# Kernel tuning notes

Measured on AMD Instinct MI355X. Metric: run time of the kernel, lower is better.

Reference implementation:

```python
import jax, jax.numpy as jnp
import numpy as np

B, IN, H, OUT = 4096, 1024, 2048, 1024
EPS = 1e-5  # added to std (not variance), matching the torch module


def _ln(z, a, b):
    # torch.std default is unbiased (ddof=1); eps added to sigma
    mu = jnp.mean(z, axis=1, keepdims=True)
    sigma = jnp.std(z, axis=1, ddof=1, keepdims=True)
    return (z - mu) / (sigma + EPS) * a + b


def setup_inputs() -> dict:
    key = jax.random.key(0)
    ks = iter(jax.random.split(key, 40))
    W = lambda i, o: (jax.random.normal(next(ks), (o, i), jnp.float32) / np.sqrt(i)).astype(jnp.float32)
    bz = lambda o: jnp.zeros((o,), jnp.float32)
    d = {
        "inp": jax.random.normal(next(ks), (B, IN), jnp.float32),
        "h_0": jax.random.normal(next(ks), (B, H), jnp.float32),
        "c_0": jax.random.normal(next(ks), (B, H), jnp.float32),
        # h-side gate linears (H -> H)
        "Wfh": W(H, H), "bfh": bz(H), "Wih": W(H, H), "bih": bz(H),
        "Wch": W(H, H), "bch": bz(H), "Woh": W(H, H), "boh": bz(H),
        # x-side gate linears (IN -> H)
        "Wfx": W(IN, H), "bfx": bz(H), "Wix": W(IN, H), "bix": bz(H),
        "Wcx": W(IN, H), "bcx": bz(H), "Wox": W(IN, H), "box": bz(H),
        # decoder (H -> OUT)
        "Wdec": W(H, OUT), "bdec": bz(OUT),
        # LayerNormalization params (a2 ones, b2 zeros), shape (1, H)
        "ax": jnp.ones((1, H), jnp.float32), "bx": jnp.zeros((1, H), jnp.float32),
        "ah": jnp.ones((1, H), jnp.float32), "bh": jnp.zeros((1, H), jnp.float32),
        "ac": jnp.ones((1, H), jnp.float32), "bc": jnp.zeros((1, H), jnp.float32),
    }
    return d


def reference(inp, h_0, c_0,
              Wfh, bfh, Wih, bih, Wch, bch, Woh, boh,
              Wfx, bfx, Wix, bix, Wcx, bcx, Wox, box,
              Wdec, bdec, ax, bx, ah, bh, ac, bc):
    lin = lambda x, W, b: x @ W.T + b
    gate = lambda wx, bx_, wh, bh_: (_ln(lin(inp, wx, bx_), ax, bx)
                                     + _ln(lin(h_0, wh, bh_), ah, bh))
    f_g = jax.nn.sigmoid(gate(Wfx, bfx, Wfh, bfh))
    i_g = jax.nn.sigmoid(gate(Wix, bix, Wih, bih))
    c_tilda = jnp.tanh(gate(Wcx, bcx, Wch, bch))
    cx = f_g * c_0 + i_g * c_tilda
    o_g = jax.nn.sigmoid(gate(Wox, box, Woh, boh))
    hx = o_g * jnp.tanh(_ln(cx, ac, bc))
    out = lin(hx, Wdec, bdec)  # decoder applied to hidden state (vectorized over batch)
    return (out, hx, cx)
```

## Files before the change

### kernel.cpp

```cpp
#include <hip/hip_runtime.h>

#define NB   4096
#define NIN  1024
#define NH   2048
#define NOUT 1024
#define NH4  8192

typedef short short8 __attribute__((ext_vector_type(8)));
typedef float f32x4 __attribute__((ext_vector_type(4)));
typedef float f32x16 __attribute__((ext_vector_type(16)));
typedef unsigned short ushort8v __attribute__((ext_vector_type(8)));

__device__ __forceinline__ float bf2f(unsigned short u) {
  union { unsigned int i; float f; } c; c.i = ((unsigned int)u) << 16; return c.f;
}
__device__ __forceinline__ unsigned short f2bf(float f) {
  union { float f; unsigned int i; } c; c.f = f;
  unsigned int u = c.i;
  u += 0x7FFFu + ((u >> 16) & 1u);
  return (unsigned short)(u >> 16);
}
__device__ __forceinline__ float sigf(float x) { return 1.0f / (1.0f + __expf(-x)); }
__device__ __forceinline__ float tanh_f(float x) { return 1.0f - 2.0f / (__expf(2.0f * x) + 1.0f); }

#define CNT_INP  ((size_t)NB * NIN)
#define CNT_H0   ((size_t)NB * NH)
#define CNT_WXG  ((size_t)NH * NIN)
#define CNT_WHG  ((size_t)NH * NH)
#define CNT_WD   ((size_t)NOUT * NH)
#define OFF_XB   ((size_t)0)
#define OFF_H0B  (OFF_XB + CNT_INP)
#define OFF_HXB  (OFF_H0B + CNT_H0)
#define OFF_WX   (OFF_HXB + CNT_H0)
#define OFF_WH   (OFF_WX + 4 * CNT_WXG)
#define OFF_WD   (OFF_WH + 4 * CNT_WHG)
#define OFF_ZX   (OFF_WD + CNT_WD)
#define OFF_ZH   (OFF_ZX + (size_t)NB * NH4)
#define CVT_TOTAL (OFF_WD + CNT_WD)

struct CvtArgs { const float* src[11]; };

__global__ __launch_bounds__(256) void cvt_all(CvtArgs a, unsigned short* __restrict__ dstBase) {
  const size_t i = ((size_t)blockIdx.x * 256 + threadIdx.x) * 8;
  if (i >= CVT_TOTAL) return;
  const size_t cnt[11] = {CNT_INP, CNT_H0, CNT_WXG, CNT_WXG, CNT_WXG, CNT_WXG,
                          CNT_WHG, CNT_WHG, CNT_WHG, CNT_WHG, CNT_WD};
  const size_t dst[11] = {OFF_XB, OFF_H0B,
                          OFF_WX, OFF_WX + CNT_WXG, OFF_WX + 2 * CNT_WXG, OFF_WX + 3 * CNT_WXG,
                          OFF_WH, OFF_WH + CNT_WHG, OFF_WH + 2 * CNT_WHG, OFF_WH + 3 * CNT_WHG,
                          OFF_WD};
  size_t base = 0;
#pragma unroll
  for (int s = 0; s < 11; s++) {
    if (i < base + cnt[s]) {
      const size_t off = i - base;
      const float* sp = a.src[s] + off;
      float4 v0 = *(const float4*)(sp);
      float4 v1 = *(const float4*)(sp + 4);
      ushort8v o;
      o[0] = f2bf(v0.x); o[1] = f2bf(v0.y); o[2] = f2bf(v0.z); o[3] = f2bf(v0.w);
      o[4] = f2bf(v1.x); o[5] = f2bf(v1.y); o[6] = f2bf(v1.z); o[7] = f2bf(v1.w);
      *(ushort8v*)(dstBase + dst[s] + off) = o;
      return;
    }
    base += cnt[s];
  }
}

__device__ __forceinline__ void gload16(const void* g, void* l) {
  __builtin_amdgcn_global_load_lds((const __attribute__((address_space(1))) void*)g,
                                   (__attribute__((address_space(3))) void*)l, 16, 0, 0);
}

#define SCH0  __builtin_amdgcn_sched_barrier(0)
#define BARR  __builtin_amdgcn_s_barrier()
#define LGKM0 asm volatile("s_waitcnt lgkmcnt(0)" ::: "memory")
#define VMC6  asm volatile("s_waitcnt vmcnt(6)" ::: "memory")
#define VMC0  asm volatile("s_waitcnt vmcnt(0)" ::: "memory")

__global__ __launch_bounds__(512) void gemm_dual8(
    const unsigned short* __restrict__ Xb, const unsigned short* __restrict__ Wx,
    const unsigned short* __restrict__ H0b, const unsigned short* __restrict__ Wh,
    const float* bx0, const float* bx1, const float* bx2, const float* bx3,
    const float* bh0, const float* bh1, const float* bh2, const float* bh3,
    unsigned short* __restrict__ Zx, unsigned short* __restrict__ Zh) {
  __shared__ __align__(16) unsigned short As[2][256 * 64];
  __shared__ __align__(16) unsigned short Bs[2][256 * 64];

  const unsigned short* Ag; const unsigned short* Bg;
  const float *p0, *p1, *p2, *p3; unsigned short* Cg; int K;
  if (blockIdx.z == 0) { Ag = Xb;  Bg = Wx; Cg = Zx; K = NIN; p0 = bx0; p1 = bx1; p2 = bx2; p3 = bx3; }
  else                 { Ag = H0b; Bg = Wh; Cg = Zh; K = NH;  p0 = bh0; p1 = bh1; p2 = bh2; p3 = bh3; }

  const int t    = threadIdx.x;
  const int wid  = t >> 6;
  const int lane = t & 63;
  const int m15  = lane & 15;
  const int g4   = lane >> 4;
  const int wm   = wid >> 2;
  const int wn   = wid & 3;
  const int rloc = lane >> 3;
  const int slot = lane & 7;
  const int ck   = slot ^ rloc ^ ((wid & 3) << 1);
  const int m0   = blockIdx.y * 256;
  const int n0   = blockIdx.x * 256;
  const int NT   = K >> 6;
  const size_t thrOff = (size_t)(wid * 8 + rloc) * K + ck * 8;

#define STAGE_HALF(G, R0, H, TT, LDBASE) do {                                                     \
    const unsigned short* _gs = (G) + thrOff + (size_t)((R0) + (H) * 128) * K + (size_t)(TT) * 64; \
    unsigned short* _ld = (LDBASE) + ((H) * 128 + wid * 8) * 64;                                   \
    gload16(_gs, _ld);                                                                             \
    gload16(_gs + (size_t)64 * K, _ld + 4096);                                                     \
  } while (0)

#define SWZ(R) (((R) & 7) ^ ((((R) >> 3) & 3) << 1))
#define LD8(S, ROW, KC) (*(const short8*)&(S)[(ROW) * 64 + (((KC) ^ SWZ(ROW)) * 8)])

  f32x4 acc[8][4];
#pragma unroll
  for (int m = 0; m < 8; m++)
#pragma unroll
    for (int n = 0; n < 4; n++)
#pragma unroll
      for (int r = 0; r < 4; r++) acc[m][n][r] = 0.f;

  STAGE_HALF(Ag, m0, 0, 0, As[0]);
  STAGE_HALF(Ag, m0, 1, 0, As[0]);
  STAGE_HALF(Bg, n0, 0, 0, Bs[0]);
  STAGE_HALF(Bg, n0, 1, 0, Bs[0]);
  STAGE_HALF(Bg, n0, 0, 1, Bs[1]);
  STAGE_HALF(Bg, n0, 1, 1, Bs[1]);
  STAGE_HALF(Ag, m0, 0, 1, As[1]);
  VMC6;
  SCH0; BARR; SCH0;

  for (int kt = 0; kt < NT; ++kt) {
    const int cur = kt & 1;
    const unsigned short* sA = As[cur];
    const unsigned short* sB = Bs[cur];
    const int tp1 = (kt + 1 < NT) ? kt + 1 : NT - 1;
    const int tp2 = (kt + 2 < NT) ? kt + 2 : NT - 1;
    short8 b[4][2], a[4][2];

#pragma unroll
    for (int n = 0; n < 2; n++) {
      const int row = wn * 64 + n * 16 + m15;
      b[n][0] = LD8(sB, row, g4);
      b[n][1] = LD8(sB, row, 4 + g4);
    }
#pragma unroll
    for (int m = 0; m < 4; m++) {
      const int row = wm * 128 + m * 16 + m15;
      a[m][0] = LD8(sA, row, g4);
      a[m][1] = LD8(sA, row, 4 + g4);
    }
    STAGE_HALF(Ag, m0, 1, tp1, As[cur ^ 1]);
    SCH0; BARR; LGKM0; SCH0;
    __builtin_amdgcn_s_setprio(1);
#pragma unroll
    for (int m = 0; m < 4; m++)
#pragma unroll
      for (int n = 0; n < 2; n++) {
        acc[m][n] = __builtin_amdgcn_mfma_f32_16x16x32_bf16(a[m][0], b[n][0], acc[m][n], 0, 0, 0);
        acc[m][n] = __builtin_amdgcn_mfma_f32_16x16x32_bf16(a[m][1], b[n][1], acc[m][n], 0, 0, 0);
      }
    __builtin_amdgcn_s_setprio(0);
    SCH0; BARR; SCH0;

#pragma unroll
    for (int n = 2; n < 4; n++) {
      const int row = wn * 64 + n * 16 + m15;
      b[n][0] = LD8(sB, row, g4);
      b[n][1] = LD8(sB, row, 4 + g4);
    }
    SCH0; BARR; LGKM0; SCH0;
    __builtin_amdgcn_s_setprio(1);
#pragma unroll
    for (int m = 0; m < 4; m++)
#pragma unroll
      for (int n = 0; n < 2; n++) {
        acc[m][2 + n] = __builtin_amdgcn_mfma_f32_16x16x32_bf16(a[m][0], b[2 + n][0], acc[m][2 + n], 0, 0, 0);
        acc[m][2 + n] = __builtin_amdgcn_mfma_f32_16x16x32_bf16(a[m][1], b[2 + n][1], acc[m][2 + n], 0, 0, 0);
      }
    __builtin_amdgcn_s_setprio(0);
    SCH0; BARR; SCH0;

#pragma unroll
    for (int m = 0; m < 4; m++) {
      const int row = wm * 128 + 64 + m * 16 + m15;
      a[m][0] = LD8(sA, row, g4);
      a[m][1] = LD8(sA, row, 4 + g4);
    }
    STAGE_HALF(Bg, n0, 0, tp2, Bs[cur]);
    SCH0; BARR; LGKM0; SCH0;
    __builtin_amdgcn_s_setprio(1);
#pragma unroll
    for (int m = 0; m < 4; m++)
#pragma unroll
      for (int n = 0; n < 2; n++) {
        acc[4 + m][n] = __builtin_amdgcn_mfma_f32_16x16x32_bf16(a[m][0], b[n][0], acc[4 + m][n], 0, 0, 0);
        acc[4 + m][n] = __builtin_amdgcn_mfma_f32_16x16x32_bf16(a[m][1], b[n][1], acc[4 + m][n], 0, 0, 0);
      }
    __builtin_amdgcn_s_setprio(0);
    SCH0; BARR; SCH0;

    STAGE_HALF(Bg, n0, 1, tp2, Bs[cur]);
    STAGE_HALF(Ag, m0, 0, tp2, As[cur]);
    SCH0; BARR; SCH0;
    __builtin_amdgcn_s_setprio(1);
#pragma unroll
    for (int m = 0; m < 4; m++)
#pragma unroll
      for (int n = 0; n < 2; n++) {
        acc[4 + m][2 + n] = __builtin_amdgcn_mfma_f32_16x16x32_bf16(a[m][0], b[2 + n][0], acc[4 + m][2 + n], 0, 0, 0);
        acc[4 + m][2 + n] = __builtin_amdgcn_mfma_f32_16x16x32_bf16(a[m][1], b[2 + n][1], acc[4 + m][2 + n], 0, 0, 0);
      }
    __builtin_amdgcn_s_setprio(0);
    VMC6;
    SCH0; BARR; SCH0;
  }

  VMC0;
  SCH0; BARR; SCH0;

  {
    unsigned short* wls = &As[0][0] + wid * (16 * 68);
    float bvn[4];
#pragma unroll
    for (int n = 0; n < 4; n++) {
      const int col = n0 + wn * 64 + n * 16 + m15;
      const float* bp = (col < 2048) ? p0 : ((col < 4096) ? p1 : ((col < 6144) ? p2 : p3));
      bvn[n] = bp[col & 2047];
    }
    const int lrow0 = lane >> 3;
    const int lcol0 = (lane & 7) * 8;
#pragma unroll
    for (int mt = 0; mt < 8; mt++) {
#pragma unroll
      for (int n = 0; n < 4; n++)
#pragma unroll
        for (int r = 0; r < 4; r++)
          wls[(g4 * 4 + r) * 68 + n * 16 + m15] = f2bf(acc[mt][n][r] + bvn[n]);
      LGKM0; SCH0;
#pragma unroll
      for (int i = 0; i < 2; i++) {
        const int lrow = i * 8 + lrow0;
        short8 v = *(const short8*)&wls[lrow * 68 + lcol0];
        *(short8*)&Cg[(size_t)(m0 + wm * 128 + mt * 16 + lrow) * NH4 + (n0 + wn * 64 + lcol0)] = v;
      }
      LGKM0; SCH0;
    }
  }
#undef STAGE_HALF
#undef SWZ
#undef LD8
}

template<int MT, bool BOUT>
__device__ __forceinline__ void gemm_core32(const unsigned short* __restrict__ A,
                                            const unsigned short* __restrict__ Bm,
                                            const float* b0p, const float* b1p,
                                            const float* b2p, const float* b3p,
                                            float* __restrict__ Cf, unsigned short* __restrict__ Cb,
                                            int N, int K) {
  constexpr int TM = MT * 64;
  __shared__ __align__(16) unsigned short As[TM * 64];
  __shared__ __align__(16) unsigned short Bs[128 * 64];
  const int t = threadIdx.x;
  const int w = t >> 6;
  const int lane = t & 63;
  const int r31 = lane & 31;
  const int hi = lane >> 5;
  const int rloc = lane >> 3;
  const int slot = lane & 7;
  const int m0 = blockIdx.y * TM;
  const int n0 = blockIdx.x * 128;
  const int wm = (w >> 1) * (MT * 32);
  const int wn = (w & 1) * 64;

  f32x16 acc[MT][2];
#pragma unroll
  for (int i = 0; i < MT; i++)
#pragma unroll
    for (int j = 0; j < 2; j++)
#pragma unroll
      for (int r = 0; r < 16; r++) acc[i][j][r] = 0.f;

  const unsigned short* AgP[2 * MT];
  unsigned short* AsP[2 * MT];
#pragma unroll
  for (int q = 0; q < 2 * MT; q++) {
    const int iss = w + 4 * q;
    const int bblk = slot ^ rloc ^ (iss & 3);
    AgP[q] = A + (size_t)(m0 + iss * 8 + rloc) * K + bblk * 8;
    AsP[q] = As + iss * 512;
  }
  const unsigned short* BgP[4];
  unsigned short* BsP[4];
#pragma unroll
  for (int q = 0; q < 4; q++) {
    const int iss = w + 4 * q;
    const int bblk = slot ^ rloc ^ (iss & 3);
    BgP[q] = Bm + (size_t)(n0 + iss * 8 + rloc) * K + bblk * 8;
    BsP[q] = Bs + iss * 512;
  }

  const int swz = (r31 & 7) ^ ((r31 >> 3) & 3);

  for (int k0 = 0; k0 < K; k0 += 64) {
#pragma unroll
    for (int q = 0; q < 2 * MT; q++) gload16(AgP[q] + k0, AsP[q]);
#pragma unroll
    for (int q = 0; q < 4; q++) gload16(BgP[q] + k0, BsP[q]);
    __syncthreads();

#pragma unroll
    for (int ks = 0; ks < 4; ks++) {
      const int phys = ((ks * 2 + hi) ^ swz) * 8;
      short8 af[MT], bf[2];
#pragma unroll
      for (int mt = 0; mt < MT; mt++) af[mt] = *(const short8*)&As[(wm + mt * 32 + r31) * 64 + phys];
#pragma unroll
      for (int jt = 0; jt < 2; jt++) bf[jt] = *(const short8*)&Bs[(wn + jt * 32 + r31) * 64 + phys];
#pragma unroll
      for (int mt = 0; mt < MT; mt++)
#pragma unroll
        for (int jt = 0; jt < 2; jt++)
          acc[mt][jt] = __builtin_amdgcn_mfma_f32_32x32x16_bf16(af[mt], bf[jt], acc[mt][jt], 0, 0, 0);
    }
    __syncthreads();
  }

#pragma unroll
  for (int mt = 0; mt < MT; mt++) {
#pragma unroll
    for (int jt = 0; jt < 2; jt++) {
      const int col = n0 + wn + jt * 32 + r31;
      const float* bp = (col < 2048) ? b0p : ((col < 4096) ? b1p : ((col < 6144) ? b2p : b3p));
      const float bv = bp[col & 2047];
      const int rowb = m0 + wm + mt * 32 + hi * 4;
#pragma unroll
      for (int reg = 0; reg < 16; reg++) {
        const int row = rowb + (reg & 3) + 8 * (reg >> 2);
        const float v = acc[mt][jt][reg] + bv;
        const size_t idx = (size_t)row * N + col;
        if (BOUT) Cb[idx] = f2bf(v);
        else      Cf[idx] = v;
      }
    }
  }
}

__global__ __launch_bounds__(256) void gemm_dec(const unsigned short* __restrict__ HXb,
                                                const unsigned short* __restrict__ Wd,
                                                const float* __restrict__ bdec,
                                                float* __restrict__ out) {
  gemm_core32<1, false>(HXb, Wd, bdec, bdec, bdec, bdec, out, nullptr, NOUT, NH);
}

__global__ __launch_bounds__(256) void ln_gates(const unsigned short* __restrict__ Zx,
                                                const unsigned short* __restrict__ Zh,
                                                const float* __restrict__ c0,
                                                const float* __restrict__ ax, const float* __restrict__ bx,
                                                const float* __restrict__ ah, const float* __restrict__ bh,
                                                const float* __restrict__ ac, const float* __restrict__ bc,
                                                float* __restrict__ out_top,
                                                unsigned short* __restrict__ hx_bf) {
  const int b = blockIdx.x;
  const int t = threadIdx.x;
  const int n = t * 8;
  const int w = t >> 6;
  const int lane = t & 63;
  const float inv_n = 1.0f / 2048.0f, inv_nm1 = 1.0f / 2047.0f;

  short8 zx[4], zh[4];
  const size_t rowoff = (size_t)b * NH4;
#pragma unroll
  for (int g = 0; g < 4; g++) {
    zx[g] = *(const short8*)(Zx + rowoff + g * NH + n);
    zh[g] = *(const short8*)(Zh + rowoff + g * NH + n);
  }

  float s[16];
#pragma unroll
  for (int g = 0; g < 4; g++) {
    float su = 0, sq = 0, su2 = 0, sq2 = 0;
#pragma unroll
    for (int j = 0; j < 8; j++) {
      float v = bf2f((unsigned short)zx[g][j]); su += v; sq += v * v;
      float u = bf2f((unsigned short)zh[g][j]); su2 += u; sq2 += u * u;
    }
    s[g * 4 + 0] = su; s[g * 4 + 1] = sq; s[g * 4 + 2] = su2; s[g * 4 + 3] = sq2;
  }
#pragma unroll
  for (int i = 0; i < 16; i++) {
    float v = s[i];
#pragma unroll
    for (int o = 32; o > 0; o >>= 1) v += __shfl_xor(v, o, 64);
    s[i] = v;
  }
  __shared__ float red[4][16];
  __shared__ float red2[4][2];
  if (lane == 0) {
#pragma unroll
    for (int i = 0; i < 16; i++) red[w][i] = s[i];
  }
  __syncthreads();
#pragma unroll
  for (int i = 0; i < 16; i++) s[i] = red[0][i] + red[1][i] + red[2][i] + red[3][i];

  float mux[4], ivx[4], muh[4], ivh[4];
#pragma unroll
  for (int g = 0; g < 4; g++) {
    mux[g] = s[g * 4 + 0] * inv_n;
    float vx = fmaxf((s[g * 4 + 1] - s[g * 4 + 0] * mux[g]) * inv_nm1, 0.0f);
    ivx[g] = 1.0f / (sqrtf(vx) + 1e-5f);
    muh[g] = s[g * 4 + 2] * inv_n;
    float vh = fmaxf((s[g * 4 + 3] - s[g * 4 + 2] * muh[g]) * inv_nm1, 0.0f);
    ivh[g] = 1.0f / (sqrtf(vh) + 1e-5f);
  }

  float axl[8], bxl[8], ahl[8], bhl[8], c0l[8];
  *(float4*)&axl[0] = *(const float4*)(ax + n); *(float4*)&axl[4] = *(const float4*)(ax + n + 4);
  *(float4*)&bxl[0] = *(const float4*)(bx + n); *(float4*)&bxl[4] = *(const float4*)(bx + n + 4);
  *(float4*)&ahl[0] = *(const float4*)(ah + n); *(float4*)&ahl[4] = *(const float4*)(ah + n + 4);
  *(float4*)&bhl[0] = *(const float4*)(bh + n); *(float4*)&bhl[4] = *(const float4*)(bh + n + 4);
  const float* c0p = c0 + (size_t)b * NH + n;
  *(float4*)&c0l[0] = *(const float4*)(c0p); *(float4*)&c0l[4] = *(const float4*)(c0p + 4);

  float cx[8], og[8];
  float cs = 0, css = 0;
#pragma unroll
  for (int j = 0; j < 8; j++) {
    float pre[4];
#pragma unroll
    for (int g = 0; g < 4; g++) {
      float vx = bf2f((unsigned short)zx[g][j]);
      float vh = bf2f((unsigned short)zh[g][j]);
      pre[g] = ((vx - mux[g]) * ivx[g]) * axl[j] + bxl[j]
             + ((vh - muh[g]) * ivh[g]) * ahl[j] + bhl[j];
    }
    float fg = sigf(pre[0]);
    float ig = sigf(pre[1]);
    float ct = tanh_f(pre[2]);
    og[j] = sigf(pre[3]);
    float c = fg * c0l[j] + ig * ct;
    cx[j] = c; cs += c; css += c * c;
  }
#pragma unroll
  for (int o = 32; o > 0; o >>= 1) { cs += __shfl_xor(cs, o, 64); css += __shfl_xor(css, o, 64); }
  if (lane == 0) { red2[w][0] = cs; red2[w][1] = css; }
  __syncthreads();
  cs = red2[0][0] + red2[1][0] + red2[2][0] + red2[3][0];
  css = red2[0][1] + red2[1][1] + red2[2][1] + red2[3][1];
  const float muc = cs * inv_n;
  const float varc = fmaxf((css - cs * muc) * inv_nm1, 0.0f);
  const float ivc = 1.0f / (sqrtf(varc) + 1e-5f);

  float acl[8], bcl[8];
  *(float4*)&acl[0] = *(const float4*)(ac + n); *(float4*)&acl[4] = *(const float4*)(ac + n + 4);
  *(float4*)&bcl[0] = *(const float4*)(bc + n); *(float4*)&bcl[4] = *(const float4*)(bc + n + 4);

  float hx[8];
#pragma unroll
  for (int j = 0; j < 8; j++)
    hx[j] = og[j] * tanh_f((cx[j] - muc) * ivc * acl[j] + bcl[j]);

  float* hx_out = out_top + (size_t)NB * NOUT + (size_t)b * NH + n;
  float* cx_out = out_top + (size_t)NB * NOUT + (size_t)NB * NH + (size_t)b * NH + n;
  float4 v;
  v.x = hx[0]; v.y = hx[1]; v.z = hx[2]; v.w = hx[3]; *(float4*)(hx_out) = v;
  v.x = hx[4]; v.y = hx[5]; v.z = hx[6]; v.w = hx[7]; *(float4*)(hx_out + 4) = v;
  v.x = cx[0]; v.y = cx[1]; v.z = cx[2]; v.w = cx[3]; *(float4*)(cx_out) = v;
  v.x = cx[4]; v.y = cx[5]; v.z = cx[6]; v.w = cx[7]; *(float4*)(cx_out + 4) = v;
  ushort8v hb;
#pragma unroll
  for (int j = 0; j < 8; j++) hb[j] = f2bf(hx[j]);
  *(ushort8v*)(hx_bf + (size_t)b * NH + n) = hb;
}

extern "C" void kernel_launch(void* const* d_in, const int* in_sizes, int n_in,
                              void* d_out, int out_size, void* d_ws, size_t ws_size,
                              hipStream_t stream) {
  const float* inp = (const float*)d_in[0];
  const float* h0  = (const float*)d_in[1];
  const float* c0  = (const float*)d_in[2];
  const float* bhg[4] = {(const float*)d_in[4], (const float*)d_in[6], (const float*)d_in[8], (const float*)d_in[10]};
  const float* bxg[4] = {(const float*)d_in[12], (const float*)d_in[14], (const float*)d_in[16], (const float*)d_in[18]};
  const float* bdec = (const float*)d_in[20];
  const float* ax = (const float*)d_in[21];
  const float* bx = (const float*)d_in[22];
  const float* ah = (const float*)d_in[23];
  const float* bh = (const float*)d_in[24];
  const float* ac = (const float*)d_in[25];
  const float* bc = (const float*)d_in[26];

  unsigned short* wsb = (unsigned short*)d_ws;
  unsigned short* Xb   = wsb + OFF_XB;
  unsigned short* H0b  = wsb + OFF_H0B;
  unsigned short* HXb  = wsb + OFF_HXB;
  unsigned short* Wx4b = wsb + OFF_WX;
  unsigned short* Wh4b = wsb + OFF_WH;
  unsigned short* Wdb  = wsb + OFF_WD;
  unsigned short* Zx   = wsb + OFF_ZX;
  unsigned short* Zh   = wsb + OFF_ZH;

  CvtArgs ca;
  ca.src[0] = inp; ca.src[1] = h0;
  ca.src[2] = (const float*)d_in[11]; ca.src[3] = (const float*)d_in[13];
  ca.src[4] = (const float*)d_in[15]; ca.src[5] = (const float*)d_in[17];
  ca.src[6] = (const float*)d_in[3];  ca.src[7] = (const float*)d_in[5];
  ca.src[8] = (const float*)d_in[7];  ca.src[9] = (const float*)d_in[9];
  ca.src[10] = (const float*)d_in[19];
  {
    const size_t nthr = CVT_TOTAL / 8;
    cvt_all<<<dim3((unsigned)((nthr + 255) / 256)), dim3(256), 0, stream>>>(ca, wsb);
  }

  gemm_dual8<<<dim3(NH4 / 256, NB / 256, 2), 512, 0, stream>>>(
      Xb, Wx4b, H0b, Wh4b,
      bxg[0], bxg[1], bxg[2], bxg[3],
      bhg[0], bhg[1], bhg[2], bhg[3],
      Zx, Zh);

  ln_gates<<<dim3(NB), 256, 0, stream>>>(Zx, Zh, c0, ax, bx, ah, bh, ac, bc, (float*)d_out, HXb);

  gemm_dec<<<dim3(NOUT / 128, NB / 64), 256, 0, stream>>>(HXb, Wdb, bdec, (float*)d_out);
}
```

Before: 578.6 us.

## Restructure dual-GEMM main loop with unroll-by-two and finer LDS/MFMA interleaving

The main K loop of gemm_dual8 is unrolled by two with fixed double-buffer indices. Swizzled LDS offsets for the A and B fragments are precomputed once per thread. Each tile step now issues LDS fragment reads in smaller groups between MFMA batches and drops several workgroup barriers and explicit lgkmcnt waits, so LDS reads overlap with matrix math. The risk is that leaving waitcnt placement to the compiler, plus keeping more fragments live at once, raises register pressure or adds hidden stalls.

```diff
diff --git a/kernel.cpp b/kernel.cpp
--- a/kernel.cpp
+++ b/kernel.cpp
@@ -77,6 +77,115 @@
 #define LGKM0 asm volatile("s_waitcnt lgkmcnt(0)" ::: "memory")
 #define VMC6  asm volatile("s_waitcnt vmcnt(6)" ::: "memory")
 #define VMC0  asm volatile("s_waitcnt vmcnt(0)" ::: "memory")
+#define PRIO1 __builtin_amdgcn_s_setprio(1)
+#define PRIO0 __builtin_amdgcn_s_setprio(0)
+#define MFMA16(A, B, C) __builtin_amdgcn_mfma_f32_16x16x32_bf16((A), (B), (C), 0, 0, 0)
+
+#define SWZ(R) (((R) & 7) ^ ((((R) >> 3) & 3) << 1))
+
+
+__device__ __forceinline__ void stage_half(const unsigned short* __restrict__ G, size_t thrOff, int K,
+                                           int R0, int H, int T, unsigned short* __restrict__ ldbase, int wid) {
+  const unsigned short* gs = G + thrOff + (size_t)(R0 + H * 128) * K + (size_t)T * 64;
+  unsigned short* ld = ldbase + (H * 128 + wid * 8) * 64;
+  gload16(gs, ld);
+  gload16(gs + (size_t)64 * K, ld + 4096);
+}
+
+__device__ __forceinline__ void tile_step(
+    const unsigned short* __restrict__ sA, const unsigned short* __restrict__ sB,
+    unsigned short* __restrict__ sAc, unsigned short* __restrict__ sBc, unsigned short* __restrict__ sAn,
+    int t1, int t2,
+    const unsigned short* __restrict__ Ag, const unsigned short* __restrict__ Bg,
+    size_t thrOff, int m0, int n0, int K, int wid,
+    const int (&oA)[8][2], const int (&oB)[4][2], f32x4 (&acc)[8][4]) {
+  short8 b01[2][2], b23[2][2], alo[4][2], ahi[4][2];
+
+#pragma unroll
+  for (int n = 0; n < 2; n++) {
+    b01[n][0] = *(const short8*)&sB[oB[n][0]];
+    b01[n][1] = *(const short8*)&sB[oB[n][1]];
+  }
+#pragma unroll
+  for (int m = 0; m < 2; m++) {
+    alo[m][0] = *(const short8*)&sA[oA[m][0]];
+    alo[m][1] = *(const short8*)&sA[oA[m][1]];
+  }
+  stage_half(Ag, thrOff, K, m0, 1, t1, sAn, wid);
+  SCH0;
+#pragma unroll
+  for (int m = 2; m < 4; m++) {
+    alo[m][0] = *(const short8*)&sA[oA[m][0]];
+    alo[m][1] = *(const short8*)&sA[oA[m][1]];
+  }
+  SCH0;
+  PRIO1;
+#pragma unroll
+  for (int m = 0; m < 2; m++)
+#pragma unroll
+    for (int n = 0; n < 2; n++) {
+      acc[m][n] = MFMA16(alo[m][0], b01[n][0], acc[m][n]);
+      acc[m][n] = MFMA16(alo[m][1], b01[n][1], acc[m][n]);
+    }
+  PRIO0; SCH0;
+#pragma unroll
+  for (int n = 0; n < 2; n++) {
+    b23[n][0] = *(const short8*)&sB[oB[2 + n][0]];
+    b23[n][1] = *(const short8*)&sB[oB[2 + n][1]];
+  }
+  SCH0;
+  PRIO1;
+#pragma unroll
+  for (int m = 2; m < 4; m++)
+#pragma unroll
+    for (int n = 0; n < 2; n++) {
+      acc[m][n] = MFMA16(alo[m][0], b01[n][0], acc[m][n]);
+      acc[m][n] = MFMA16(alo[m][1], b01[n][1], acc[m][n]);
+    }
+  PRIO0; SCH0;
+#pragma unroll
+  for (int m = 0; m < 4; m++) {
+    ahi[m][0] = *(const short8*)&sA[oA[4 + m][0]];
+    ahi[m][1] = *(const short8*)&sA[oA[4 + m][1]];
+  }
+  SCH0;
+  PRIO1;
+#pragma unroll
+  for (int m = 0; m < 4; m++)
+#pragma unroll
+    for (int n = 0; n < 2; n++) {
+      acc[m][2 + n] = MFMA16(alo[m][0], b23[n][0], acc[m][2 + n]);
+      acc[m][2 + n] = MFMA16(alo[m][1], b23[n][1], acc[m][2 + n]);
+    }
+  PRIO0;
+  SCH0; BARR; SCH0;
+  stage_half(Bg, thrOff, K, n0, 0, t2, sBc, wid);
+  stage_half(Bg, thrOff, K, n0, 1, t2, sBc, wid);
+  SCH0;
+  PRIO1;
+#pragma unroll
+  for (int m = 0; m < 4; m++)
+#pragma unroll
+    for (int n = 0; n < 2; n++) {
+      acc[4 + m][n] = MFMA16(ahi[m][0], b01[n][0], acc[4 + m][n]);
+      acc[4 + m][n] = MFMA16(ahi[m][1], b01[n][1], acc[4 + m][n]);
+    }
+  PRIO0;
+  SCH0; BARR; SCH0;
+  stage_half(Ag, thrOff, K, m0, 0, t2, sAc, wid);
+  SCH0;
+  PRIO1;
+#pragma unroll
+  for (int m = 0; m < 4; m++)
+#pragma unroll
+    for (int n = 0; n < 2; n++) {
+      acc[4 + m][2 + n] = MFMA16(ahi[m][0], b23[n][0], acc[4 + m][2 + n]);
+      acc[4 + m][2 + n] = MFMA16(ahi[m][1], b23[n][1], acc[4 + m][2 + n]);
+    }
+  PRIO0;
+  VMC6;
+  SCH0; BARR; SCH0;
+}
 
 __global__ __launch_bounds__(512) void gemm_dual8(
     const unsigned short* __restrict__ Xb, const unsigned short* __restrict__ Wx,
@@ -107,15 +216,23 @@
   const int NT   = K >> 6;
   const size_t thrOff = (size_t)(wid * 8 + rloc) * K + ck * 8;
 
-#define STAGE_HALF(G, R0, H, TT, LDBASE) do {                                                     \
-    const unsigned short* _gs = (G) + thrOff + (size_t)((R0) + (H) * 128) * K + (size_t)(TT) * 64; \
-    unsigned short* _ld = (LDBASE) + ((H) * 128 + wid * 8) * 64;                                   \
-    gload16(_gs, _ld);                                                                             \
-    gload16(_gs + (size_t)64 * K, _ld + 4096);                                                     \
-  } while (0)
-
-#define SWZ(R) (((R) & 7) ^ ((((R) >> 3) & 3) << 1))
-#define LD8(S, ROW, KC) (*(const short8*)&(S)[(ROW) * 64 + (((KC) ^ SWZ(ROW)) * 8)])
+  int oA[8][2], oB[4][2];
+#pragma unroll
+  for (int m = 0; m < 4; m++) {
+    const int r1 = wm * 128 + m * 16 + m15;
+    const int r2 = r1 + 64;
+#pragma unroll
+    for (int h = 0; h < 2; h++) {
+      oA[m][h]     = r1 * 64 + (((h * 4 + g4) ^ SWZ(r1)) * 8);
+      oA[4 + m][h] = r2 * 64 + (((h * 4 + g4) ^ SWZ(r2)) * 8);
+    }
+  }
+#pragma unroll
+  for (int n = 0; n < 4; n++) {
+    const int r = wn * 64 + n * 16 + m15;
+#pragma unroll
+    for (int h = 0; h < 2; h++) oB[n][h] = r * 64 + (((h * 4 + g4) ^ SWZ(r)) * 8);
+  }
 
   f32x4 acc[8][4];
 #pragma unroll
@@ -125,100 +242,24 @@
 #pragma unroll
       for (int r = 0; r < 4; r++) acc[m][n][r] = 0.f;
 
-  STAGE_HALF(Ag, m0, 0, 0, As[0]);
-  STAGE_HALF(Ag, m0, 1, 0, As[0]);
-  STAGE_HALF(Bg, n0, 0, 0, Bs[0]);
-  STAGE_HALF(Bg, n0, 1, 0, Bs[0]);
-  STAGE_HALF(Bg, n0, 0, 1, Bs[1]);
-  STAGE_HALF(Bg, n0, 1, 1, Bs[1]);
-  STAGE_HALF(Ag, m0, 0, 1, As[1]);
+  stage_half(Ag, thrOff, K, m0, 0, 0, As[0], wid);
+  stage_half(Ag, thrOff, K, m0, 1, 0, As[0], wid);
+  stage_half(Bg, thrOff, K, n0, 0, 0, Bs[0], wid);
+  stage_half(Bg, thrOff, K, n0, 1, 0, Bs[0], wid);
+  stage_half(Bg, thrOff, K, n0, 0, 1, Bs[1], wid);
+  stage_half(Bg, thrOff, K, n0, 1, 1, Bs[1], wid);
+  stage_half(Ag, thrOff, K, m0, 0, 1, As[1], wid);
   VMC6;
   SCH0; BARR; SCH0;
 
-  for (int kt = 0; kt < NT; ++kt) {
-    const int cur = kt & 1;
-    const unsigned short* sA = As[cur];
-    const unsigned short* sB = Bs[cur];
-    const int tp1 = (kt + 1 < NT) ? kt + 1 : NT - 1;
-    const int tp2 = (kt + 2 < NT) ? kt + 2 : NT - 1;
-    short8 b[4][2], a[4][2];
-
-#pragma unroll
-    for (int n = 0; n < 2; n++) {
-      const int row = wn * 64 + n * 16 + m15;
-      b[n][0] = LD8(sB, row, g4);
-      b[n][1] = LD8(sB, row, 4 + g4);
-    }
-#pragma unroll
-    for (int m = 0; m < 4; m++) {
-      const int row = wm * 128 + m * 16 + m15;
-      a[m][0] = LD8(sA, row, g4);
-      a[m][1] = LD8(sA, row, 4 + g4);
-    }
-    STAGE_HALF(Ag, m0, 1, tp1, As[cur ^ 1]);
-    SCH0; BARR; LGKM0; SCH0;
-    __builtin_amdgcn_s_setprio(1);
-#pragma unroll
-    for (int m = 0; m < 4; m++)
-#pragma unroll
-      for (int n = 0; n < 2; n++) {
-        acc[m][n] = __builtin_amdgcn_mfma_f32_16x16x32_bf16(a[m][0], b[n][0], acc[m][n], 0, 0, 0);
-        acc[m][n] = __builtin_amdgcn_mfma_f32_16x16x32_bf16(a[m][1], b[n][1], acc[m][n], 0, 0, 0);
-      }
-    __builtin_amdgcn_s_setprio(0);
-    SCH0; BARR; SCH0;
-
-#pragma unroll
-    for (int n = 2; n < 4; n++) {
-      const int row = wn * 64 + n * 16 + m15;
-      b[n][0] = LD8(sB, row, g4);
-      b[n][1] = LD8(sB, row, 4 + g4);
-    }
-    SCH0; BARR; LGKM0; SCH0;
-    __builtin_amdgcn_s_setprio(1);
-#pragma unroll
-    for (int m = 0; m < 4; m++)
-#pragma unroll
-      for (int n = 0; n < 2; n++) {
-        acc[m][2 + n] = __builtin_amdgcn_mfma_f32_16x16x32_bf16(a[m][0], b[2 + n][0], acc[m][2 + n], 0, 0, 0);
-        acc[m][2 + n] = __builtin_amdgcn_mfma_f32_16x16x32_bf16(a[m][1], b[2 + n][1], acc[m][2 + n], 0, 0, 0);
-      }
-    __builtin_amdgcn_s_setprio(0);
-    SCH0; BARR; SCH0;
-
-#pragma unroll
-    for (int m = 0; m < 4; m++) {
-      const int row = wm * 128 + 64 + m * 16 + m15;
-      a[m][0] = LD8(sA, row, g4);
-      a[m][1] = LD8(sA, row, 4 + g4);
-    }
-    STAGE_HALF(Bg, n0, 0, tp2, Bs[cur]);
-    SCH0; BARR; LGKM0; SCH0;
-    __builtin_amdgcn_s_setprio(1);
-#pragma unroll
-    for (int m = 0; m < 4; m++)
-#pragma unroll
-      for (int n = 0; n < 2; n++) {
-        acc[4 + m][n] = __builtin_amdgcn_mfma_f32_16x16x32_bf16(a[m][0], b[n][0], acc[4 + m][n], 0, 0, 0);
-        acc[4 + m][n] = __builtin_amdgcn_mfma_f32_16x16x32_bf16(a[m][1], b[n][1], acc[4 + m][n], 0, 0, 0);
-      }
-    __builtin_amdgcn_s_setprio(0);
-    SCH0; BARR; SCH0;
-
-    STAGE_HALF(Bg, n0, 1, tp2, Bs[cur]);
-    STAGE_HALF(Ag, m0, 0, tp2, As[cur]);
-    SCH0; BARR; SCH0;
-    __builtin_amdgcn_s_setprio(1);
-#pragma unroll
-    for (int m = 0; m < 4; m++)
-#pragma unroll
-      for (int n = 0; n < 2; n++) {
-        acc[4 + m][2 + n] = __builtin_amdgcn_mfma_f32_16x16x32_bf16(a[m][0], b[2 + n][0], acc[4 + m][2 + n], 0, 0, 0);
-        acc[4 + m][2 + n] = __builtin_amdgcn_mfma_f32_16x16x32_bf16(a[m][1], b[2 + n][1], acc[4 + m][2 + n], 0, 0, 0);
-      }
-    __builtin_amdgcn_s_setprio(0);
-    VMC6;
-    SCH0; BARR; SCH0;
+  for (int kt = 0; kt < NT; kt += 2) {
+    const int t2a = (kt + 2 < NT) ? kt + 2 : NT - 1;
+    const int t1b = t2a;
+    const int t2b = (kt + 3 < NT) ? kt + 3 : NT - 1;
+    tile_step(As[0], Bs[0], As[0], Bs[0], As[1], kt + 1, t2a,
+              Ag, Bg, thrOff, m0, n0, K, wid, oA, oB, acc);
+    tile_step(As[1], Bs[1], As[1], Bs[1], As[0], t1b, t2b,
+              Ag, Bg, thrOff, m0, n0, K, wid, oA, oB, acc);
   }
 
   VMC0;
@@ -252,9 +293,6 @@
       LGKM0; SCH0;
     }
   }
-#undef STAGE_HALF
-#undef SWZ
-#undef LD8
 }
 
 template<int MT, bool BOUT>
```

Result: faster. 561.5 us (-2.9%).
